# Performance work log

Measured on AMD Instinct MI355X. Metric: run time of the kernel, lower is better.

The kernel has to match this reference:

```python
import jax, jax.numpy as jnp
import numpy as np
from jax import lax

H = 1024      # hidden_size
E = 512       # embedding_size
K = 4         # max_num_children
NCLASS = 10000
EOS = NCLASS
N = 256       # number of tree nodes (complete K-ary tree, topo order)
L = 512       # number of annotation vectors


def setup_inputs() -> dict:
    key = jax.random.key(0)
    ks = jax.random.split(key, 16)
    s = 0.05
    rootH = jax.random.normal(ks[0], (1, H), jnp.float32)
    rootC = jax.random.normal(ks[1], (1, H), jnp.float32)
    annotations = jax.random.normal(ks[2], (L, H), jnp.float32)
    values = jax.random.randint(ks[3], (N,), 0, NCLASS, jnp.int32)
    idx = np.arange(N)
    parent = jnp.asarray(np.maximum(idx - 1, 0) // K, jnp.int32)
    slot = jnp.asarray(np.maximum(idx - 1, 0) % K, jnp.int32)
    # learned parameters
    emb = jax.random.normal(ks[4], (NCLASS + 1, E), jnp.float32) * s
    W_ih = jax.random.normal(ks[5], (K, 4 * H, E + H), jnp.float32) * s
    W_hh = jax.random.normal(ks[6], (K, 4 * H, H), jnp.float32) * s
    b_ih = jax.random.normal(ks[7], (K, 4 * H), jnp.float32) * s
    b_hh = jax.random.normal(ks[8], (K, 4 * H), jnp.float32) * s
    W_att = jax.random.normal(ks[9], (H, H), jnp.float32) * s
    b_att = jax.random.normal(ks[10], (H,), jnp.float32) * s
    W_pre = jax.random.normal(ks[11], (H, 2 * H), jnp.float32) * s
    b_pre = jax.random.normal(ks[12], (H,), jnp.float32) * s
    W_out = jax.random.normal(ks[13], (NCLASS + 1, H), jnp.float32) * s
    b_out = jax.random.normal(ks[14], (NCLASS + 1,), jnp.float32) * s
    return dict(rootH=rootH, rootC=rootC, annotations=annotations, values=values,
                parent=parent, slot=slot, emb=emb, W_ih=W_ih, W_hh=W_hh,
                b_ih=b_ih, b_hh=b_hh, W_att=W_att, b_att=b_att,
                W_pre=W_pre, b_pre=b_pre, W_out=W_out, b_out=b_out)


def reference(rootH, rootC, annotations, values, parent, slot, emb,
              W_ih, W_hh, b_ih, b_hh, W_att, b_att, W_pre, b_pre, W_out, b_out):
    # attention_hidden(annotations), computed once (align_type=1)
    ahv = annotations @ W_att.T + b_att            # [L, H]
    rootH0, rootC0 = rootH[0], rootC[0]            # [H]

    def step(carry, xs):
        Hbuf, Cbuf, etbuf, loss = carry
        i, v, p, k = xs
        # child LSTMCell update from parent state (slot k picks the cell)
        x = jnp.concatenate([emb[values[p]], etbuf[p]])            # [E+H]
        gates = W_ih[k] @ x + b_ih[k] + W_hh[k] @ Hbuf[p] + b_hh[k]  # [4H]
        ig, fg, gg, og = jnp.split(gates, 4)
        c_child = jax.nn.sigmoid(fg) * Cbuf[p] + jax.nn.sigmoid(ig) * jnp.tanh(gg)
        h_child = jax.nn.sigmoid(og) * jnp.tanh(c_child)
        is_root = i == 0
        h = jnp.where(is_root, rootH0, h_child)
        c = jnp.where(is_root, rootC0, c_child)
        # attention over annotations (softmax over L)
        att_logits = ahv @ h                                        # [L]
        probs = jax.nn.softmax(att_logits)
        ctx = probs @ annotations                                   # [H]
        et = jnp.tanh(W_pre @ jnp.concatenate([h, ctx]) + b_pre)    # [H]
        # output: softmax then CrossEntropyLoss (faithful double softmax)
        out_logits = W_out @ et + b_out                             # [NCLASS+1]
        p_out = jax.nn.softmax(out_logits)
        ls = jax.nn.log_softmax(p_out)
        nl = -ls[v]
        nl = jnp.where(v == EOS, nl / 5.0, nl)
        Hbuf = Hbuf.at[i].set(h)
        Cbuf = Cbuf.at[i].set(c)
        etbuf = etbuf.at[i].set(et)
        return (Hbuf, Cbuf, etbuf, loss + nl), None

    z = jnp.zeros((N, H), jnp.float32)
    init = (z, z, z, jnp.float32(0.0))
    xs = (jnp.arange(N, dtype=jnp.int32), values, parent, slot)
    (Hb, Cb, eb, loss), _ = lax.scan(step, init, xs)
    return loss
```

## Files before the change

### kernel.cpp

```cpp
#include <hip/hip_runtime.h>
#include <hip/hip_bf16.h>
#include <math.h>

#define HD 1024
#define NCLS 10001

typedef short s16x8 __attribute__((ext_vector_type(8)));
typedef unsigned short u16x8 __attribute__((ext_vector_type(8)));
typedef unsigned short u16x4 __attribute__((ext_vector_type(4)));
typedef float f32x4 __attribute__((ext_vector_type(4)));
#define MFMA16(a_, b_, c_) __builtin_amdgcn_mfma_f32_16x16x32_bf16((a_), (b_), (c_), 0, 0, 0)

__device__ __forceinline__ float sigf(float x){ return 1.f/(1.f+__expf(-x)); }
__device__ __forceinline__ float tanhfast(float x){
  x = fminf(fmaxf(x,-10.f),10.f);
  float e2 = __expf(2.f*x);
  return (e2-1.f)/(e2+1.f);
}
__device__ __forceinline__ unsigned short f2bf(float f){
  unsigned int u = __float_as_uint(f);
  u += 0x7FFF + ((u >> 16) & 1);
  return (unsigned short)(u >> 16);
}
__device__ __forceinline__ float bf2f(unsigned short u){
  return __uint_as_float(((unsigned)u) << 16);
}
__device__ __forceinline__ u16x8 pack8(float4 a, float4 b){
  u16x8 r;
  r[0]=f2bf(a.x); r[1]=f2bf(a.y); r[2]=f2bf(a.z); r[3]=f2bf(a.w);
  r[4]=f2bf(b.x); r[5]=f2bf(b.y); r[6]=f2bf(b.z); r[7]=f2bf(b.w);
  return r;
}

__global__ __launch_bounds__(256) void k_cvtall(
    const float* __restrict__ Wih, const float* __restrict__ Whh,
    const float* __restrict__ ann, const float* __restrict__ Watt, const float* __restrict__ Wpre,
    unsigned short* __restrict__ Wbih, unsigned short* __restrict__ Wbhh,
    unsigned short* __restrict__ Annb, unsigned short* __restrict__ Wattb,
    unsigned short* __restrict__ Bpre, unsigned short* __restrict__ Wpcb)
{
  const int b = blockIdx.x;
  if (b >= 5312) {
    unsigned base = (unsigned)(b-5312)*8192u;
    #pragma unroll
    for (int it=0; it<4; ++it) {
      unsigned idx = base + ((unsigned)it*256u + threadIdx.x)*8u;
      const float* sp = Wpre + idx;
      unsigned row = idx >> 11, c = idx & 2047;
      unsigned short* dp = (c < 1024) ? (Bpre + (size_t)row*1536 + c) : (Wpcb + (size_t)row*1024 + (c-1024));
      float4 a = *(const float4*)sp, bb = *(const float4*)(sp+4);
      *(u16x8*)dp = pack8(a,bb);
    }
    return;
  }
  const float* src; unsigned short* dst;
  if (b < 3072)      { unsigned o=(unsigned)b*8192u;        src=Wih+o;  dst=Wbih+o; }
  else if (b < 5120) { unsigned o=(unsigned)(b-3072)*8192u; src=Whh+o;  dst=Wbhh+o; }
  else if (b < 5184) { unsigned o=(unsigned)(b-5120)*8192u; src=ann+o;  dst=Annb+o; }
  else               { unsigned o=(unsigned)(b-5184)*8192u; src=Watt+o; dst=Wattb+o; }

  const unsigned t8 = threadIdx.x*8u;
  float4 a0 = *(const float4*)(src +        t8), b0 = *(const float4*)(src +        t8 + 4);
  float4 a1 = *(const float4*)(src + 2048 + t8), b1 = *(const float4*)(src + 2048 + t8 + 4);
  float4 a2 = *(const float4*)(src + 4096 + t8), b2 = *(const float4*)(src + 4096 + t8 + 4);
  float4 a3 = *(const float4*)(src + 6144 + t8), b3 = *(const float4*)(src + 6144 + t8 + 4);
  asm volatile("" :: "v"(a0.x), "v"(b0.x), "v"(a1.x), "v"(b1.x),
                     "v"(a2.x), "v"(b2.x), "v"(a3.x), "v"(b3.x));
  *(u16x8*)(dst +        t8) = pack8(a0,b0);
  *(u16x8*)(dst + 2048 + t8) = pack8(a1,b1);
  *(u16x8*)(dst + 4096 + t8) = pack8(a2,b2);
  *(u16x8*)(dst + 6144 + t8) = pack8(a3,b3);
}

__global__ __launch_bounds__(64) void k_emb(const float* __restrict__ emb, const int* __restrict__ values,
                                            unsigned short* __restrict__ Xb){
  int i = blockIdx.x + 1;
  int lev, s;
  if (i < 5)       { lev=1; s=1; }
  else if (i < 21) { lev=2; s=5; }
  else if (i < 85) { lev=3; s=21; }
  else             { lev=4; s=85; }
  int p = (i-1)>>2, o = i - s;
  unsigned short* xr = Xb + ((size_t)(lev-1)*4*48 + (size_t)(o&3)*48 + (o>>2)) * 2560;
  const float* er = emb + (size_t)values[p]*512;
  int c = threadIdx.x*8;
  float4 a = *(const float4*)(er+c), b = *(const float4*)(er+c+4);
  *(u16x8*)(xr+c) = pack8(a,b);
}

__global__ __launch_bounds__(256) void k_root(const float* __restrict__ rH, const float* __restrict__ rC,
                                              float* __restrict__ Cb, unsigned short* __restrict__ XH,
                                              unsigned short* __restrict__ Xb1){
  int u = threadIdx.x*4;
  float4 h = *(const float4*)(rH+u);
  float4 c = *(const float4*)(rC+u);
  *(float4*)(Cb+u) = c;
  u16x4 r; r[0]=f2bf(h.x); r[1]=f2bf(h.y); r[2]=f2bf(h.z); r[3]=f2bf(h.w);
  *(u16x4*)(XH+u) = r;
  #pragma unroll
  for (int k=0;k<4;++k)
    *(u16x4*)(Xb1 + (size_t)k*48*2560 + 1536 + u) = r;
}

template<int MT>
__global__ __launch_bounds__(256) void k_gemm_fb(
    const unsigned short* __restrict__ A, int astride,
    const unsigned short* __restrict__ B, int K,
    const float* __restrict__ bias,
    unsigned short* __restrict__ Cb16,
    int ostride, int coff, int N, int M)
{
  const int mb0 = blockIdx.y * (MT*16);
  const int wv = threadIdx.x >> 6, lane = threadIdx.x & 63;
  const int col = (blockIdx.x*4 + wv)*16 + (lane & 15);
  const int colc = min(col, N-1);
  const int khalf = (lane >> 4) * 8;

  f32x4 acc[MT];
  #pragma unroll
  for (int m = 0; m < MT; ++m) acc[m] = (f32x4){0.f,0.f,0.f,0.f};
  int arow[MT];
  #pragma unroll
  for (int m = 0; m < MT; ++m) arow[m] = min(mb0 + m*16 + (lane & 15), M-1);

  #pragma unroll 4
  for (int kk = 0; kk < K; kk += 32) {
    int kb = kk + khalf;
    s16x8 bfv = *(const s16x8*)(B + (size_t)colc*K + kb);
    #pragma unroll
    for (int m = 0; m < MT; ++m) {
      s16x8 af = *(const s16x8*)(A + (size_t)arow[m]*astride + kb);
      acc[m] = MFMA16(af, bfv, acc[m]);
    }
  }

  const int r0 = (lane >> 4) * 4;
  #pragma unroll
  for (int m = 0; m < MT; ++m) {
    #pragma unroll
    for (int q = 0; q < 4; ++q) {
      int row = mb0 + m*16 + r0 + q;
      if (row < M && col < N) {
        float v = acc[m][q] + (bias ? bias[col] : 0.f);
        Cb16[(size_t)row*ostride + col + coff] = f2bf(v);
      }
    }
  }
}

__global__ __launch_bounds__(256) void k_wout(
    const unsigned short* __restrict__ A,
    const float* __restrict__ B,
    const float* __restrict__ bias,
    unsigned short* __restrict__ Lgb)
{
  __shared__ unsigned short bs[16*1032];
  const int c0 = blockIdx.x*16;
  const int tid = threadIdx.x;
  #pragma unroll
  for (int it = 0; it < 8; ++it) {
    int e = it*2048 + tid*8;
    int row = e >> 10, ck = e & 1023;
    int rr = min(c0 + row, NCLS-1);
    const float* sp = B + (size_t)rr*1024 + ck;
    float4 a = *(const float4*)sp, b = *(const float4*)(sp+4);
    *(u16x8*)(bs + row*1032 + ck) = pack8(a,b);
  }
  __syncthreads();

  const int wv = tid >> 6, lane = tid & 63;
  const int col16 = lane & 15;
  const int khalf = (lane >> 4) * 8;
  const int mb0 = wv * 64;
  const int col = c0 + col16;

  f32x4 acc[4];
  #pragma unroll
  for (int m=0;m<4;++m) acc[m] = (f32x4){0.f,0.f,0.f,0.f};
  int arow[4];
  #pragma unroll
  for (int m=0;m<4;++m) arow[m] = mb0 + m*16 + col16;

  #pragma unroll 8
  for (int kk = 0; kk < 1024; kk += 32) {
    int kb = kk + khalf;
    s16x8 bfv = *(const s16x8*)(bs + col16*1032 + kb);
    #pragma unroll
    for (int m=0;m<4;++m) {
      s16x8 af = *(const s16x8*)(A + (size_t)arow[m]*1024 + kb);
      acc[m] = MFMA16(af, bfv, acc[m]);
    }
  }

  if (col < NCLS) {
    const int r0 = (lane >> 4) * 4;
    float bv = bias[col];
    #pragma unroll
    for (int m=0;m<4;++m) {
      #pragma unroll
      for (int q=0;q<4;++q) {
        int row = mb0 + m*16 + r0 + q;
        Lgb[(size_t)row*NCLS + col] = f2bf(acc[m][q] + bv);
      }
    }
  }
}

template<int MT, int KITER>
__global__ __launch_bounds__(256) void k_gemm_skzb2(
    const unsigned short* __restrict__ A, int astride,
    const unsigned short* __restrict__ B1, int K1,
    const unsigned short* __restrict__ B2, int K2,
    float* __restrict__ P, int N, int Mbase, int Mpad,
    int aZ, int b1Z, int b2Z, int KS)
{
  const int z = blockIdx.z;
  const int M = (Mbase - z + 3) >> 2;
  const unsigned short* Az = A + (size_t)z*aZ;
  const unsigned short* B1z = B1 + (size_t)z*b1Z;
  const unsigned short* B2z = B2 + (size_t)z*b2Z;
  const int ks = blockIdx.y;
  const int k0 = ks * (KITER*32);
  const int wv = threadIdx.x >> 6, lane = threadIdx.x & 63;
  const int col = (blockIdx.x*4 + wv)*16 + (lane & 15);
  const int colc = min(col, N-1);
  const int khalf = (lane >> 4) * 8;

  f32x4 acc[MT];
  #pragma unroll
  for (int m = 0; m < MT; ++m) acc[m] = (f32x4){0.f,0.f,0.f,0.f};
  int arow[MT];
  #pragma unroll
  for (int m = 0; m < MT; ++m) arow[m] = min(m*16 + (lane & 15), M-1);

  #pragma unroll 8
  for (int kk = 0; kk < KITER*32; kk += 32) {
    int kb = k0 + kk + khalf;
    const unsigned short* bp = (kb < K1) ? (B1z + (size_t)colc*K1 + kb)
                                         : (B2z + (size_t)colc*K2 + (kb - K1));
    s16x8 bfv = *(const s16x8*)bp;
    #pragma unroll
    for (int m = 0; m < MT; ++m) {
      s16x8 af = *(const s16x8*)(Az + (size_t)arow[m]*astride + kb);
      acc[m] = MFMA16(af, bfv, acc[m]);
    }
  }

  const int r0 = (lane >> 4) * 4;
  #pragma unroll
  for (int m = 0; m < MT; ++m) {
    #pragma unroll
    for (int q = 0; q < 4; ++q) {
      int row = m*16 + r0 + q;
      if (row < M && col < N)
        P[(((size_t)z*KS + ks)*Mpad + row)*N + col] = acc[m][q];
    }
  }
}

template<int MT>
__global__ __launch_bounds__(256) void k_gemm_skb(
    const unsigned short* __restrict__ A, int astride,
    const unsigned short* __restrict__ B, int K,
    float* __restrict__ P, int N, int M)
{
  const int ks = blockIdx.y;
  const int k0 = ks * 128;
  const int wv = threadIdx.x >> 6, lane = threadIdx.x & 63;
  const int col = (blockIdx.x*4 + wv)*16 + (lane & 15);
  const int colc = min(col, N-1);
  const int khalf = (lane >> 4) * 8;

  f32x4 acc[MT];
  #pragma unroll
  for (int m = 0; m < MT; ++m) acc[m] = (f32x4){0.f,0.f,0.f,0.f};
  int arow[MT];
  #pragma unroll
  for (int m = 0; m < MT; ++m) arow[m] = min(m*16 + (lane & 15), M-1);

  #pragma unroll
  for (int kk = 0; kk < 128; kk += 32) {
    int kb = k0 + kk + khalf;
    s16x8 bfv = *(const s16x8*)(B + (size_t)colc*K + kb);
    #pragma unroll
    for (int m = 0; m < MT; ++m) {
      s16x8 af = *(const s16x8*)(A + (size_t)arow[m]*astride + kb);
      acc[m] = MFMA16(af, bfv, acc[m]);
    }
  }

  const int r0 = (lane >> 4) * 4;
  #pragma unroll
  for (int m = 0; m < MT; ++m) {
    #pragma unroll
    for (int q = 0; q < 4; ++q) {
      int row = m*16 + r0 + q;
      if (row < M && col < N)
        P[((size_t)ks*M + row)*N + col] = acc[m][q];
    }
  }
}

__global__ __launch_bounds__(256) void k_soft(const float* __restrict__ P, int KS, int M,
                                              unsigned short* __restrict__ dst)
{
  __shared__ float sm[512];
  __shared__ float red[8];
  const int m = blockIdx.x;
  const int tid = threadIdx.x, wv = tid>>6, ln = tid&63;
  for (int l = tid; l < 512; l += 256) {
    float s = 0.f;
    for (int ks = 0; ks < KS; ++ks) s += P[((size_t)ks*M + m)*512 + l];
    sm[l] = s;
  }
  __syncthreads();
  float mx = -1e30f;
  for (int l=tid; l<512; l+=256) mx = fmaxf(mx, sm[l]);
  #pragma unroll
  for (int o=32;o;o>>=1) mx = fmaxf(mx, __shfl_xor(mx,o,64));
  if (ln==0) red[wv]=mx;
  __syncthreads();
  mx = fmaxf(fmaxf(red[0],red[1]),fmaxf(red[2],red[3]));
  float se = 0.f;
  for (int l=tid; l<512; l+=256){ float ev=__expf(sm[l]-mx); sm[l]=ev; se+=ev; }
  __syncthreads();
  #pragma unroll
  for (int o=32;o;o>>=1) se += __shfl_xor(se,o,64);
  if (ln==0) red[wv]=se;
  __syncthreads();
  float invS = 1.f/(red[0]+red[1]+red[2]+red[3]);
  for (int l=tid; l<512; l+=256) dst[(size_t)m*1536 + l] = f2bf(sm[l]*invS);
}

__global__ __launch_bounds__(256) void k_red4(const float* __restrict__ P, int KS, int M,
                                              const float* __restrict__ bias,
                                              unsigned short* __restrict__ Etb, int s,
                                              int snext, unsigned short* __restrict__ XbNext)
{
  const int row = blockIdx.x;
  const int col = threadIdx.x*4;
  float4 sum = *(const float4*)(bias + col);
  for (int ks = 0; ks < KS; ++ks) {
    float4 p = *(const float4*)(P + ((size_t)ks*M + row)*1024 + col);
    sum.x += p.x; sum.y += p.y; sum.z += p.z; sum.w += p.w;
  }
  u16x4 r;
  r[0]=f2bf(tanhfast(sum.x)); r[1]=f2bf(tanhfast(sum.y));
  r[2]=f2bf(tanhfast(sum.z)); r[3]=f2bf(tanhfast(sum.w));
  *(u16x4*)(Etb + (size_t)(s+row)*1024 + col) = r;
  if (XbNext) {
    int cbase = 4*(s+row) + 1;
    #pragma unroll
    for (int k=0;k<4;++k) {
      int cn = cbase + k;
      if (cn < 256) {
        int o = cn - snext;
        *(u16x4*)(XbNext + ((size_t)(o&3)*48 + (o>>2))*2560 + 512 + col) = r;
      }
    }
  }
}

__global__ __launch_bounds__(256) void k_epi(const float* __restrict__ P,
                                             const float* __restrict__ b_ih, const float* __restrict__ b_hh,
                                             float* __restrict__ Cb, unsigned short* __restrict__ XH,
                                             int s, int snext, unsigned short* __restrict__ XbNext){
  int i = s + blockIdx.x;
  int slot = (i - s) & 3, j = (i - s) >> 2;
  int p = (i - 1) >> 2;
  const float* bi = b_ih + (size_t)slot*4096;
  const float* bh = b_hh + (size_t)slot*4096;
  const int u = threadIdx.x*4;

  float4 ig, fg, gg, og;
  {
    float4 a, b;
    a = *(const float4*)(bi+u);      b = *(const float4*)(bh+u);      ig = make_float4(a.x+b.x,a.y+b.y,a.z+b.z,a.w+b.w);
    a = *(const float4*)(bi+1024+u); b = *(const float4*)(bh+1024+u); fg = make_float4(a.x+b.x,a.y+b.y,a.z+b.z,a.w+b.w);
    a = *(const float4*)(bi+2048+u); b = *(const float4*)(bh+2048+u); gg = make_float4(a.x+b.x,a.y+b.y,a.z+b.z,a.w+b.w);
    a = *(const float4*)(bi+3072+u); b = *(const float4*)(bh+3072+u); og = make_float4(a.x+b.x,a.y+b.y,a.z+b.z,a.w+b.w);
  }
  #pragma unroll
  for (int ks = 0; ks < 5; ++ks) {
    const float* g = P + (((size_t)slot*5 + ks)*48 + j)*4096;
    float4 a;
    a = *(const float4*)(g+u);      ig.x+=a.x; ig.y+=a.y; ig.z+=a.z; ig.w+=a.w;
    a = *(const float4*)(g+1024+u); fg.x+=a.x; fg.y+=a.y; fg.z+=a.z; fg.w+=a.w;
    a = *(const float4*)(g+2048+u); gg.x+=a.x; gg.y+=a.y; gg.z+=a.z; gg.w+=a.w;
    a = *(const float4*)(g+3072+u); og.x+=a.x; og.y+=a.y; og.z+=a.z; og.w+=a.w;
  }
  float4 cp = *(const float4*)(Cb + (size_t)p*1024 + u);
  float4 cc, hh;
  cc.x = sigf(fg.x)*cp.x + sigf(ig.x)*tanhfast(gg.x); hh.x = sigf(og.x)*tanhfast(cc.x);
  cc.y = sigf(fg.y)*cp.y + sigf(ig.y)*tanhfast(gg.y); hh.y = sigf(og.y)*tanhfast(cc.y);
  cc.z = sigf(fg.z)*cp.z + sigf(ig.z)*tanhfast(gg.z); hh.z = sigf(og.z)*tanhfast(cc.z);
  cc.w = sigf(fg.w)*cp.w + sigf(ig.w)*tanhfast(gg.w); hh.w = sigf(og.w)*tanhfast(cc.w);
  *(float4*)(Cb + (size_t)i*1024 + u) = cc;
  u16x4 r; r[0]=f2bf(hh.x); r[1]=f2bf(hh.y); r[2]=f2bf(hh.z); r[3]=f2bf(hh.w);
  *(u16x4*)(XH + (size_t)i*1536 + u) = r;
  if (XbNext) {
    int cbase = 4*i + 1;
    #pragma unroll
    for (int k=0;k<4;++k) {
      int cn = cbase + k;
      if (cn < 256) {
        int o = cn - snext;
        *(u16x4*)(XbNext + ((size_t)(o&3)*48 + (o>>2))*2560 + 1536 + u) = r;
      }
    }
  }
}

__global__ __launch_bounds__(256) void k_loss(const unsigned short* __restrict__ Lgb,
                                              const int* __restrict__ values,
                                              float* __restrict__ Nl)
{
  __shared__ float red[8];
  const int node = blockIdx.x;
  const int tid = threadIdx.x, wv = tid>>6, ln = tid&63;
  const unsigned short* lg = Lgb + (size_t)node*NCLS;

  u16x8 v0 = *(const u16x8*)(lg + 0*2048 + tid*8);
  u16x8 v1 = *(const u16x8*)(lg + 1*2048 + tid*8);
  u16x8 v2 = *(const u16x8*)(lg + 2*2048 + tid*8);
  u16x8 v3 = *(const u16x8*)(lg + 3*2048 + tid*8);
  u16x8 v4;
  {
    int e = 8192 + tid*8;
    #pragma unroll
    for (int k=0;k<8;++k) v4[k] = (e+k < NCLS) ? lg[e+k] : (unsigned short)0xFF80;
  }

  float m = -1e30f;
  #pragma unroll
  for (int k=0;k<8;++k){
    m = fmaxf(m, bf2f(v0[k])); m = fmaxf(m, bf2f(v1[k]));
    m = fmaxf(m, bf2f(v2[k])); m = fmaxf(m, bf2f(v3[k]));
    m = fmaxf(m, bf2f(v4[k]));
  }
  #pragma unroll
  for (int o=32;o;o>>=1) m = fmaxf(m, __shfl_xor(m,o,64));
  if (ln==0) red[wv]=m;
  __syncthreads();
  m = fmaxf(fmaxf(red[0],red[1]),fmaxf(red[2],red[3]));
  __syncthreads();

  float s = 0.f;
  #pragma unroll
  for (int k=0;k<8;++k){
    s += __expf(bf2f(v0[k])-m); s += __expf(bf2f(v1[k])-m);
    s += __expf(bf2f(v2[k])-m); s += __expf(bf2f(v3[k])-m);
    s += __expf(bf2f(v4[k])-m);
  }
  #pragma unroll
  for (int o=32;o;o>>=1) s += __shfl_xor(s,o,64);
  if (ln==0) red[wv]=s;
  __syncthreads();
  s = red[0]+red[1]+red[2]+red[3];
  __syncthreads();
  float invs = 1.f/s;

  float q = 0.f;
  #pragma unroll
  for (int k=0;k<8;++k){
    q += __expf(__expf(bf2f(v0[k])-m)*invs);
    q += __expf(__expf(bf2f(v1[k])-m)*invs);
    q += __expf(__expf(bf2f(v2[k])-m)*invs);
    q += __expf(__expf(bf2f(v3[k])-m)*invs);
    if (8192 + tid*8 + k < NCLS) q += __expf(__expf(bf2f(v4[k])-m)*invs);
  }
  #pragma unroll
  for (int o=32;o;o>>=1) q += __shfl_xor(q,o,64);
  if (ln==0) red[wv]=q;
  __syncthreads();
  if (tid==0) {
    float qq = red[0]+red[1]+red[2]+red[3];
    int v = values[node];
    float pv = __expf(bf2f(lg[v])-m)*invs;
    float nl = __logf(qq) - pv;
    if (v == NCLS-1) nl *= 0.2f;
    Nl[node] = nl;
  }
}

__global__ __launch_bounds__(256) void k_final(const float* __restrict__ Nl, float* __restrict__ out){
  __shared__ float red[8];
  int tid = threadIdx.x, wv = tid>>6, ln = tid&63;
  float s = Nl[tid];
  #pragma unroll
  for (int o=32;o;o>>=1) s += __shfl_xor(s,o,64);
  if (ln==0) red[wv]=s;
  __syncthreads();
  if (tid==0) out[0] = red[0]+red[1]+red[2]+red[3];
}

static inline void gemm_skb(hipStream_t st, int MT, const unsigned short* A, int astride,
                            const unsigned short* B, int K, float* P, int N, int M)
{
  dim3 grid(N/64, K/128);
  #define SKCASE(MTv) k_gemm_skb<MTv><<<grid, 256, 0, st>>>(A,astride,B,K,P,N,M)
  switch(MT){
    case 1:  SKCASE(1);  break;
    case 4:  SKCASE(4);  break;
    case 11: SKCASE(11); break;
    default: SKCASE(16); break;
  }
  #undef SKCASE
}

extern "C" void kernel_launch(void* const* d_in, const int* in_sizes, int n_in,
                              void* d_out, int out_size, void* d_ws, size_t ws_size,
                              hipStream_t stream)
{
  const float* rootH = (const float*)d_in[0];
  const float* rootC = (const float*)d_in[1];
  const float* ann   = (const float*)d_in[2];
  const int*   values= (const int*)d_in[3];
  const float* emb   = (const float*)d_in[6];
  const float* W_ih  = (const float*)d_in[7];
  const float* W_hh  = (const float*)d_in[8];
  const float* b_ih  = (const float*)d_in[9];
  const float* b_hh  = (const float*)d_in[10];
  const float* W_att = (const float*)d_in[11];
  const float* b_att = (const float*)d_in[12];
  const float* W_pre = (const float*)d_in[13];
  const float* b_pre = (const float*)d_in[14];
  const float* W_out = (const float*)d_in[15];
  const float* b_out = (const float*)d_in[16];

  float* ws = (float*)d_ws;
  float* Cb  = ws; ws += 256*1024;
  float* Nl  = ws; ws += 256;
  float* PB  = ws; ws += 4*5*48*4096;
  unsigned short* Wbih  = (unsigned short*)ws;
  unsigned short* Wbhh  = Wbih  + (size_t)4*4096*1536;
  unsigned short* Wattb = Wbhh  + (size_t)4*4096*1024;
  unsigned short* Bpre  = Wattb + 1024*1024;
  unsigned short* Wpcb  = Bpre  + 1024*1536;
  unsigned short* AHVb  = Wpcb  + 1024*1024;
  unsigned short* Annb  = AHVb  + 512*1024;
  unsigned short* XH    = Annb  + 512*1024;
  unsigned short* Etb   = XH    + 256*1536;
  unsigned short* Xb    = Etb   + 256*1024;
  unsigned short* Lgb   = Xb    + (size_t)4*4*48*2560;

  k_cvtall<<<5568, 256, 0, stream>>>(W_ih, W_hh, ann, W_att, W_pre,
                                     Wbih, Wbhh, Annb, Wattb, Bpre, Wpcb);
  k_emb   <<<255,  64,  0, stream>>>(emb, values, Xb);
  k_gemm_fb<4><<<dim3(16,8), 256, 0, stream>>>(Annb, 1024, Wattb, 1024, b_att, AHVb, 1024, 0, 1024, 512);
  k_gemm_fb<4><<<dim3(8,16), 256, 0, stream>>>(Wpcb, 1024, Annb, 1024, nullptr, Bpre, 1536, 1024, 512, 1024);
  k_root<<<1, 256, 0, stream>>>(rootH, rootC, Cb, XH, Xb);

  const int LS[6] = {0,1,5,21,85,256};
  for (int lev=0; lev<5; ++lev){
    int s=LS[lev], e=LS[lev+1], n=e-s;
    unsigned short* XbL = Xb + (size_t)(lev-1)*4*48*2560;
    unsigned short* XbN = (lev<4) ? (Xb + (size_t)lev*4*48*2560) : nullptr;
    int snext = (lev<4) ? LS[lev+1] : 0;
    if (lev>0){
      if (lev==4)
        k_gemm_skzb2<3,16><<<dim3(64,5,4),256,0,stream>>>(XbL, 2560, Wbih, 1536, Wbhh, 1024, PB,
            4096, n, 48, 48*2560, 4096*1536, 4096*1024, 5);
      else
        k_gemm_skzb2<1,16><<<dim3(64,5,4),256,0,stream>>>(XbL, 2560, Wbih, 1536, Wbhh, 1024, PB,
            4096, n, 48, 48*2560, 4096*1536, 4096*1024, 5);
      k_epi<<<n,256,0,stream>>>(PB, b_ih, b_hh, Cb, XH, s, snext, XbN);
    }
    int mtn = (n+15)/16;
    gemm_skb(stream, mtn, XH + (size_t)s*1536, 1536, AHVb, 1024, PB, 512, n);
    k_soft<<<n,256,0,stream>>>(PB, 8, n, XH + (size_t)s*1536 + 1024);
    gemm_skb(stream, mtn, XH + (size_t)s*1536, 1536, Bpre, 1536, PB, 1024, n);
    k_red4<<<n,256,0,stream>>>(PB, 12, n, b_pre, Etb, s, snext, XbN);
  }

  k_wout<<<626, 256, 0, stream>>>(Etb, W_out, b_out, Lgb);
  k_loss <<<256,256,0,stream>>>(Lgb, values, Nl);
  k_final<<<1,  256,0,stream>>>(Nl, (float*)d_out);
}
```

Before: 397.6 us.

## Fuse LSTM weight bf16 conversion into first-level gate GEMM

```diff
diff --git a/kernel.cpp b/kernel.cpp
--- a/kernel.cpp
+++ b/kernel.cpp
@@ -31,17 +31,19 @@
   r[4]=f2bf(b.x); r[5]=f2bf(b.y); r[6]=f2bf(b.z); r[7]=f2bf(b.w);
   return r;
 }
-
-__global__ __launch_bounds__(256) void k_cvtall(
-    const float* __restrict__ Wih, const float* __restrict__ Whh,
+__device__ __forceinline__ float4 ntload4(const float* p){
+  f32x4 v = __builtin_nontemporal_load((const f32x4*)p);
+  return make_float4(v[0], v[1], v[2], v[3]);
+}
+
+__global__ __launch_bounds__(256) void k_cvtsmall(
     const float* __restrict__ ann, const float* __restrict__ Watt, const float* __restrict__ Wpre,
-    unsigned short* __restrict__ Wbih, unsigned short* __restrict__ Wbhh,
     unsigned short* __restrict__ Annb, unsigned short* __restrict__ Wattb,
     unsigned short* __restrict__ Bpre, unsigned short* __restrict__ Wpcb)
 {
   const int b = blockIdx.x;
-  if (b >= 5312) {
-    unsigned base = (unsigned)(b-5312)*8192u;
+  if (b >= 192) {
+    unsigned base = (unsigned)(b-192)*8192u;
     #pragma unroll
     for (int it=0; it<4; ++it) {
       unsigned idx = base + ((unsigned)it*256u + threadIdx.x)*8u;
@@ -54,22 +56,15 @@
     return;
   }
   const float* src; unsigned short* dst;
-  if (b < 3072)      { unsigned o=(unsigned)b*8192u;        src=Wih+o;  dst=Wbih+o; }
-  else if (b < 5120) { unsigned o=(unsigned)(b-3072)*8192u; src=Whh+o;  dst=Wbhh+o; }
-  else if (b < 5184) { unsigned o=(unsigned)(b-5120)*8192u; src=ann+o;  dst=Annb+o; }
-  else               { unsigned o=(unsigned)(b-5184)*8192u; src=Watt+o; dst=Wattb+o; }
-
+  if (b < 64) { unsigned o=(unsigned)b*8192u;      src=ann+o;  dst=Annb+o; }
+  else        { unsigned o=(unsigned)(b-64)*8192u; src=Watt+o; dst=Wattb+o; }
   const unsigned t8 = threadIdx.x*8u;
-  float4 a0 = *(const float4*)(src +        t8), b0 = *(const float4*)(src +        t8 + 4);
-  float4 a1 = *(const float4*)(src + 2048 + t8), b1 = *(const float4*)(src + 2048 + t8 + 4);
-  float4 a2 = *(const float4*)(src + 4096 + t8), b2 = *(const float4*)(src + 4096 + t8 + 4);
-  float4 a3 = *(const float4*)(src + 6144 + t8), b3 = *(const float4*)(src + 6144 + t8 + 4);
-  asm volatile("" :: "v"(a0.x), "v"(b0.x), "v"(a1.x), "v"(b1.x),
-                     "v"(a2.x), "v"(b2.x), "v"(a3.x), "v"(b3.x));
-  *(u16x8*)(dst +        t8) = pack8(a0,b0);
-  *(u16x8*)(dst + 2048 + t8) = pack8(a1,b1);
-  *(u16x8*)(dst + 4096 + t8) = pack8(a2,b2);
-  *(u16x8*)(dst + 6144 + t8) = pack8(a3,b3);
+  #pragma unroll
+  for (int it=0; it<4; ++it) {
+    float4 a = *(const float4*)(src + it*2048 + t8);
+    float4 bb = *(const float4*)(src + it*2048 + t8 + 4);
+    *(u16x8*)(dst + it*2048 + t8) = pack8(a,bb);
+  }
 }
 
 __global__ __launch_bounds__(64) void k_emb(const float* __restrict__ emb, const int* __restrict__ values,
@@ -163,7 +158,8 @@
     int row = e >> 10, ck = e & 1023;
     int rr = min(c0 + row, NCLS-1);
     const float* sp = B + (size_t)rr*1024 + ck;
-    float4 a = *(const float4*)sp, b = *(const float4*)(sp+4);
+    float4 a = ntload4(sp);
+    float4 b = ntload4(sp+4);
     *(u16x8*)(bs + row*1032 + ck) = pack8(a,b);
   }
   __syncthreads();
@@ -204,6 +200,46 @@
       }
     }
   }
+}
+
+__global__ __launch_bounds__(256) void k_lstm1c(
+    const unsigned short* __restrict__ A,
+    const float* __restrict__ B1f, const float* __restrict__ B2f,
+    unsigned short* __restrict__ W1, unsigned short* __restrict__ W2,
+    float* __restrict__ P)
+{
+  const int z = blockIdx.z;
+  const unsigned short* Az = A + (size_t)z*48*2560;
+  const float* B1z = B1f + (size_t)z*4096*1536;
+  const float* B2z = B2f + (size_t)z*4096*1024;
+  unsigned short* W1z = W1 + (size_t)z*4096*1536;
+  unsigned short* W2z = W2 + (size_t)z*4096*1024;
+  const int ks = blockIdx.y;
+  const int k0 = ks * 512;
+  const int wv = threadIdx.x >> 6, lane = threadIdx.x & 63;
+  const int col = (blockIdx.x*4 + wv)*16 + (lane & 15);
+  const int khalf = (lane >> 4) * 8;
+
+  f32x4 acc = (f32x4){0.f,0.f,0.f,0.f};
+  #pragma unroll 4
+  for (int kk = 0; kk < 512; kk += 32) {
+    int kb = k0 + kk + khalf;
+    const float* bp; unsigned short* wp;
+    if (kb < 1536) { bp = B1z + (size_t)col*1536 + kb;        wp = W1z + (size_t)col*1536 + kb; }
+    else           { bp = B2z + (size_t)col*1024 + (kb-1536); wp = W2z + (size_t)col*1024 + (kb-1536); }
+    float4 b0 = ntload4(bp);
+    float4 b1 = ntload4(bp+4);
+    u16x8 w = pack8(b0,b1);
+    *(u16x8*)wp = w;
+    s16x8 bfv;
+    #pragma unroll
+    for (int t=0;t<8;++t) bfv[t] = (short)w[t];
+    s16x8 af = *(const s16x8*)(Az + kb);
+    acc = MFMA16(af, bfv, acc);
+  }
+  const int r0 = (lane >> 4) * 4;
+  if (r0 == 0)
+    P[(((size_t)z*5 + ks)*48)*4096 + col] = acc[0];
 }
 
 template<int MT, int KITER>
@@ -544,8 +580,7 @@
   unsigned short* Xb    = Etb   + 256*1024;
   unsigned short* Lgb   = Xb    + (size_t)4*4*48*2560;
 
-  k_cvtall<<<5568, 256, 0, stream>>>(W_ih, W_hh, ann, W_att, W_pre,
-                                     Wbih, Wbhh, Annb, Wattb, Bpre, Wpcb);
+  k_cvtsmall<<<448, 256, 0, stream>>>(ann, W_att, W_pre, Annb, Wattb, Bpre, Wpcb);
   k_emb   <<<255,  64,  0, stream>>>(emb, values, Xb);
   k_gemm_fb<4><<<dim3(16,8), 256, 0, stream>>>(Annb, 1024, Wattb, 1024, b_att, AHVb, 1024, 0, 1024, 512);
   k_gemm_fb<4><<<dim3(8,16), 256, 0, stream>>>(Wpcb, 1024, Annb, 1024, nullptr, Bpre, 1536, 1024, 512, 1024);
@@ -557,7 +592,10 @@
     unsigned short* XbL = Xb + (size_t)(lev-1)*4*48*2560;
     unsigned short* XbN = (lev<4) ? (Xb + (size_t)lev*4*48*2560) : nullptr;
     int snext = (lev<4) ? LS[lev+1] : 0;
-    if (lev>0){
+    if (lev==1){
+      k_lstm1c<<<dim3(64,5,4),256,0,stream>>>(XbL, W_ih, W_hh, Wbih, Wbhh, PB);
+      k_epi<<<n,256,0,stream>>>(PB, b_ih, b_hh, Cb, XH, s, snext, XbN);
+    } else if (lev>1){
       if (lev==4)
         k_gemm_skzb2<3,16><<<dim3(64,5,4),256,0,stream>>>(XbL, 2560, Wbih, 1536, Wbhh, 1024, PB,
             4096, n, 48, 48*2560, 4096*1536, 4096*1024, 5);
```

After: 395.5 us. No clear change (-0.5%).
